# Optimization experiments

Measured on AMD Instinct MI355X. Metric: run time of the kernel, lower is better.

The kernel has to match this reference:

```python
import jax, jax.numpy as jnp
import numpy as np
from jax import lax

B, L, E, K = 16, 512, 512, 3
LOG_SQRT_2PI = 0.5 * float(np.log(2.0 * np.pi))


def conv1d_same(x, w, b):
    # x: (B, L, 1) -> (B, L, E); w: (E, 1, K), same padding for K=3
    y = lax.conv_general_dilated(x.transpose(0, 2, 1), w, (1,), [((K - 1) // 2, (K - 1) // 2)],
                                 dimension_numbers=('NCH', 'OIH', 'NCH'))
    return y.transpose(0, 2, 1) + b


def setup_inputs() -> dict:
    key = jax.random.key(0)
    ks = jax.random.split(key, 12)
    x = jax.random.normal(ks[0], (B, L, E), dtype=jnp.float32)
    durations_int = jax.random.randint(ks[1], (B, L), 1, 9, dtype=jnp.int32)
    durations_float = durations_int.astype(jnp.float32) + 0.1 * jax.random.normal(ks[2], (B, L), dtype=jnp.float32)
    energies = jax.random.normal(ks[3], (B, L), dtype=jnp.float32)
    pitch = jax.random.normal(ks[4], (B, L), dtype=jnp.float32)
    input_lengths = jax.random.randint(ks[5], (B,), 384, 513, dtype=jnp.int32).at[0].set(L)
    # number of frames = max total duration (data-dependent, fixed at setup time)
    T = int(np.max(np.cumsum(np.asarray(durations_int), axis=1)))
    frames_idx = jnp.arange(T, dtype=jnp.float32) + 0.5
    s = 0.02
    w_dur = s * jax.random.normal(ks[6], (E, 1, K), dtype=jnp.float32)
    b_dur = jnp.zeros((E,), dtype=jnp.float32)
    w_nrg = s * jax.random.normal(ks[7], (E, 1, K), dtype=jnp.float32)
    b_nrg = jnp.zeros((E,), dtype=jnp.float32)
    w_pitch = s * jax.random.normal(ks[8], (E, 1, K), dtype=jnp.float32)
    b_pitch = jnp.zeros((E,), dtype=jnp.float32)
    w_proj = s * jax.random.normal(ks[9], (1, E), dtype=jnp.float32)
    b_proj = jnp.zeros((1,), dtype=jnp.float32)
    return dict(x=x, durations_float=durations_float, durations_int=durations_int,
                energies=energies, pitch=pitch, input_lengths=input_lengths,
                frames_idx=frames_idx, w_dur=w_dur, b_dur=b_dur, w_nrg=w_nrg,
                b_nrg=b_nrg, w_pitch=w_pitch, b_pitch=b_pitch, w_proj=w_proj, b_proj=b_proj)


def reference(x, durations_float, durations_int, energies, pitch, input_lengths,
              frames_idx, w_dur, b_dur, w_nrg, b_nrg, w_pitch, b_pitch, w_proj, b_proj):
    dur = conv1d_same(durations_float[..., None], w_dur, b_dur)   # (B,L,E)
    nrg = conv1d_same(energies[..., None], w_nrg, b_nrg)          # (B,L,E)
    pit = conv1d_same(pitch[..., None], w_pitch, b_pitch)         # (B,L,E)
    xc = x + nrg + pit                                            # x_combined == x_summed (no concat)
    range_in = xc + dur
    ranges = jax.nn.softplus(jnp.einsum('ble,oe->blo', range_in, w_proj) + b_proj)[..., 0]  # (B,L)
    pad = jnp.arange(x.shape[1])[None, :] >= input_lengths[:, None]  # True on padded phonemes
    ranges = jnp.clip(jnp.where(pad, 1.0, ranges), 0.001)
    d = durations_int.astype(x.dtype)
    csum = jnp.cumsum(d, axis=1)
    means = d * 0.5 + (csum - d)                                   # center of each phoneme span
    stds = ranges
    # Gaussian log prob over frame centers, (B,L,T)
    z = (frames_idx[None, None, :] - means[..., None]) / stds[..., None]
    probs = jnp.exp(-0.5 * z * z - jnp.log(stds)[..., None] - LOG_SQRT_2PI)
    probs = jnp.where(pad[..., None], 0.0, probs)
    weights = probs / (jnp.sum(probs, axis=1, keepdims=True) + 1e-20)  # normalize over phonemes
    x_upsamp = jnp.einsum('ble,blt->bte', xc, weights)                 # (B,T,E)
    return x_upsamp, weights
```

## Files before the change

### kernel.cpp

```cpp
#include <hip/hip_runtime.h>

typedef unsigned short u16;
typedef unsigned int u32;
typedef __attribute__((ext_vector_type(8))) short short8;
typedef __attribute__((ext_vector_type(4))) float f32x4;

#define LOG_SQRT_2PI 0.9189385332046727f
#define NB 16
#define NL 512
#define NE 512
#define ZWIN 20.0f
#define MAXTB 32

__device__ __forceinline__ u16 f2bf(float x) {
    u32 u = __builtin_bit_cast(u32, x);
    u += 0x7fffu + ((u >> 16) & 1u);
    return (u16)(u >> 16);
}

__device__ __forceinline__ void gload_lds16(const u16* g, u16* l) {
    __builtin_amdgcn_global_load_lds(
        (__attribute__((address_space(1))) void*)(u16*)g,
        (__attribute__((address_space(3))) void*)l,
        16, 0, 0);
}

__global__ void k_xc(const float* __restrict__ x, const float* __restrict__ en,
                     const float* __restrict__ pt,
                     const float* __restrict__ wn, const float* __restrict__ bn,
                     const float* __restrict__ wq, const float* __restrict__ bq,
                     const float* __restrict__ wproj,
                     u16* __restrict__ XcT, float* __restrict__ dot8) {
    __shared__ u16 tile[64][68];
    int b = blockIdx.z;
    int l0 = blockIdx.y * 64, e0 = blockIdx.x * 64;
    int tid = threadIdx.x;
    int c16 = tid & 15, rg = tid >> 4;
    int e = e0 + c16 * 4;
    float wnA[12], wqA[12], bias[4], wp[4];
    {
        const float4* p = (const float4*)(wn + (size_t)e * 3);
        float4 a0 = p[0], a1 = p[1], a2 = p[2];
        wnA[0]=a0.x; wnA[1]=a0.y; wnA[2]=a0.z; wnA[3]=a0.w; wnA[4]=a1.x; wnA[5]=a1.y;
        wnA[6]=a1.z; wnA[7]=a1.w; wnA[8]=a2.x; wnA[9]=a2.y; wnA[10]=a2.z; wnA[11]=a2.w;
        const float4* q = (const float4*)(wq + (size_t)e * 3);
        float4 b0 = q[0], b1 = q[1], b2 = q[2];
        wqA[0]=b0.x; wqA[1]=b0.y; wqA[2]=b0.z; wqA[3]=b0.w; wqA[4]=b1.x; wqA[5]=b1.y;
        wqA[6]=b1.z; wqA[7]=b1.w; wqA[8]=b2.x; wqA[9]=b2.y; wqA[10]=b2.z; wqA[11]=b2.w;
        float4 bn4 = *(const float4*)(bn + e);
        float4 bq4 = *(const float4*)(bq + e);
        bias[0]=bn4.x+bq4.x; bias[1]=bn4.y+bq4.y; bias[2]=bn4.z+bq4.z; bias[3]=bn4.w+bq4.w;
        float4 wp4 = *(const float4*)(wproj + e);
        wp[0]=wp4.x; wp[1]=wp4.y; wp[2]=wp4.z; wp[3]=wp4.w;
    }
    int base = b * NL;
    #pragma unroll
    for (int it = 0; it < 4; ++it) {
        int ll = rg + 16 * it;
        int l = l0 + ll;
        float em1 = (l > 0)   ? en[base + l - 1] : 0.f;
        float ev  = en[base + l];
        float ep1 = (l < 511) ? en[base + l + 1] : 0.f;
        float pm1 = (l > 0)   ? pt[base + l - 1] : 0.f;
        float pv  = pt[base + l];
        float pp1 = (l < 511) ? pt[base + l + 1] : 0.f;
        float4 xv = *(const float4*)(x + ((size_t)(base + l)) * NE + e);
        float xa[4] = {xv.x, xv.y, xv.z, xv.w};
        float pd = 0.f;
        #pragma unroll
        for (int k = 0; k < 4; ++k) {
            float v = xa[k]
                    + wnA[k*3+0] * em1 + wnA[k*3+1] * ev + wnA[k*3+2] * ep1
                    + wqA[k*3+0] * pm1 + wqA[k*3+1] * pv + wqA[k*3+2] * pp1 + bias[k];
            tile[ll][c16 * 4 + k] = f2bf(v);
            pd = fmaf(v, wp[k], pd);
        }
        #pragma unroll
        for (int m = 8; m; m >>= 1) pd += __shfl_xor(pd, m);
        if (c16 == 0) dot8[((size_t)(base + l)) * 8 + blockIdx.x] = pd;
    }
    __syncthreads();
    int lr = tid >> 6, c = tid & 63;
    #pragma unroll 4
    for (int it = 0; it < 16; ++it) {
        int eo = lr + 4 * it;
        XcT[((size_t)b * NE + (e0 + eo)) * NL + l0 + c] = tile[c][eo];
    }
}

__global__ void k_pre(const int* __restrict__ dint, const float* __restrict__ df,
                      const int* __restrict__ lens,
                      const float* __restrict__ wproj, const float* __restrict__ wd,
                      const float* __restrict__ bd, const float* __restrict__ bproj,
                      const float* __restrict__ dot8,
                      float* __restrict__ means, float* __restrict__ inv_std,
                      float* __restrict__ Aarr, int2* __restrict__ win, int ntb) {
    int b = blockIdx.x, l = threadIdx.x;
    __shared__ float s[NL];
    __shared__ float red[4][8];
    __shared__ float tarr[4];
    __shared__ int slo[MAXTB], shi[MAXTB];
    {
        float wp = wproj[l];
        float v[4] = {wp * wd[l * 3 + 0], wp * wd[l * 3 + 1], wp * wd[l * 3 + 2], wp * bd[l]};
        int lane = l & 63, wv = l >> 6;
        #pragma unroll
        for (int i = 0; i < 4; i++) {
            float t = v[i];
            for (int m = 32; m; m >>= 1) t += __shfl_xor(t, m);
            if (lane == 0) red[i][wv] = t;
        }
    }
    if (l < ntb) { slo[l] = NL; shi[l] = -1; }
    float d = (float)dint[b * NL + l];
    s[l] = d;
    __syncthreads();
    if (l < 4) {
        float t = 0.f;
        for (int w2 = 0; w2 < 8; w2++) t += red[l][w2];
        if (l == 3) t += bproj[0];
        tarr[l] = t;
    }
    for (int off = 1; off < NL; off <<= 1) {
        float v = (l >= off) ? s[l - off] : 0.0f;
        __syncthreads();
        s[l] += v;
        __syncthreads();
    }
    float mean = s[l] - 0.5f * d;
    means[b * NL + l] = mean;
    int base = b * NL;
    float dot;
    {
        const float4* dp = (const float4*)(dot8 + ((size_t)(base + l)) * 8);
        float4 a = dp[0], bb4 = dp[1];
        dot = ((a.x + a.y) + (a.z + a.w)) + ((bb4.x + bb4.y) + (bb4.z + bb4.w));
    }
    float dm1 = (l > 0)   ? df[base + l - 1] : 0.f;
    float d0  = df[base + l];
    float dp1 = (l < 511) ? df[base + l + 1] : 0.f;
    float lin = dot + tarr[3]
              + tarr[0] * dm1 + tarr[1] * d0 + tarr[2] * dp1;
    float r = (lin > 20.f) ? lin : log1pf(expf(lin));
    bool pad = (l >= lens[b]);
    if (pad) r = 1.0f;
    float sd = fmaxf(r, 0.001f);
    inv_std[base + l] = 1.0f / sd;
    Aarr[base + l] = pad ? -1e30f : (-logf(sd) - LOG_SQRT_2PI);
    if (!pad) {
        float fl = mean - ZWIN * sd - 1.0f;
        float fh = mean + ZWIN * sd + 1.0f;
        for (int tb = 0; tb < ntb; ++tb) {
            float t_lo = tb * 128.0f + 0.5f, t_hi = tb * 128.0f + 127.5f;
            if (fl <= t_hi && fh >= t_lo) {
                atomicMin(&slo[tb], l);
                atomicMax(&shi[tb], l);
            }
        }
    }
    __syncthreads();
    if (l < ntb) win[b * MAXTB + l] = make_int2(slo[l], shi[l]);
}

__global__ __launch_bounds__(256) void k_gemm(const u16* __restrict__ XcT,
                                              const float* __restrict__ frames,
                                              const float* __restrict__ means,
                                              const float* __restrict__ inv_std,
                                              const float* __restrict__ Aarr,
                                              const int2* __restrict__ win,
                                              float* __restrict__ out,
                                              float* __restrict__ wout, int T) {
    __shared__ float4 sq[NL];
    __shared__ float fts[128];
    __shared__ float part[2][128];
    __shared__ float rvs[128];
    __shared__ u16 At[2][128][32];
    __shared__ u16 Bt[2][128][32];
    int b = blockIdx.z;
    int t0 = blockIdx.y * 128;
    int e0 = blockIdx.x * 128;
    int tid = threadIdx.x;
    int lane = tid & 63, wid = tid >> 6;
    int wm = wid >> 1, wn = wid & 1;
    const u16* Bb = XcT + (size_t)b * NE * NL;

    int2 w = win[b * MAXTB + blockIdx.y];
    int ks0 = 0, nst = 0;
    if (w.x <= w.y) { ks0 = w.x >> 5; nst = (w.y >> 5) - ks0 + 1; }
    int bl0 = ks0 * 32, bl1 = (ks0 + nst) * 32;

    for (int i = bl0 + tid; i < bl1; i += 256)
        sq[i] = make_float4(means[b * NL + i], inv_std[b * NL + i], Aarr[b * NL + i], 0.f);
    if (tid < 128) fts[tid] = (t0 + tid < T) ? frames[t0 + tid] : -1e9f;

    __syncthreads();

    if (nst > 0) {
        int tr = tid & 127, h = tid >> 7;
        float ftr = fts[tr];
        float ssum = 0.f;
        for (int l = w.x + h; l <= w.y; l += 2) {
            float4 q = sq[l];
            float z = (ftr - q.x) * q.y;
            ssum += __expf(fmaf(z, -0.5f * z, q.z));
        }
        part[h][tr] = ssum;
    }
    __syncthreads();
    if (tid < 128) rvs[tid] = 1.0f / (part[0][tid] + part[1][tid] + 1e-20f);
    __syncthreads();

    int ta = tid >> 1;
    int ha = (tid & 1) * 16;
    float ft = fts[ta];
    float rv = rvs[ta];

    int srow = wid * 32 + (lane >> 2);
    int skc = (lane & 3) * 8;

    f32x4 acc[4][4];
    #pragma unroll
    for (int m = 0; m < 4; m++)
        #pragma unroll
        for (int n = 0; n < 4; n++)
            #pragma unroll
            for (int k = 0; k < 4; k++) acc[m][n][k] = 0.0f;

    auto stage = [&](int buf, int ks) {
        int l0 = ks * 32;
        const u16* gb = Bb + (size_t)(e0 + srow) * NL + l0 + skc;
        gload_lds16(gb, &Bt[buf][wid * 32][0]);
        gload_lds16(gb + 16 * NL, &Bt[buf][wid * 32 + 16][0]);
        u32 pk[8];
        #pragma unroll
        for (int jj = 0; jj < 8; ++jj) {
            float4 q0 = sq[l0 + ha + jj * 2];
            float4 q1 = sq[l0 + ha + jj * 2 + 1];
            float z0 = (ft - q0.x) * q0.y;
            float p0 = __expf(fmaf(z0, -0.5f * z0, q0.z)) * rv;
            float z1 = (ft - q1.x) * q1.y;
            float p1 = __expf(fmaf(z1, -0.5f * z1, q1.z)) * rv;
            pk[jj] = (u32)f2bf(p0) | ((u32)f2bf(p1) << 16);
        }
        *(uint4*)&At[buf][ta][ha]     = make_uint4(pk[0], pk[1], pk[2], pk[3]);
        *(uint4*)&At[buf][ta][ha + 8] = make_uint4(pk[4], pk[5], pk[6], pk[7]);
    };

    int fr = lane & 15, fk = (lane >> 4) * 8;
    if (nst > 0) {
        stage(0, ks0);
        for (int s = 0; s < nst; ++s) {
            __syncthreads();
            if (s + 1 < nst) stage((s + 1) & 1, ks0 + s + 1);
            int buf = s & 1;
            short8 a[4], bb[4];
            #pragma unroll
            for (int m = 0; m < 4; m++)
                a[m] = *(const short8*)&At[buf][wm * 64 + m * 16 + fr][fk];
            #pragma unroll
            for (int n = 0; n < 4; n++)
                bb[n] = *(const short8*)&Bt[buf][wn * 64 + n * 16 + fr][fk];
            #pragma unroll
            for (int m = 0; m < 4; m++)
                #pragma unroll
                for (int n = 0; n < 4; n++)
                    acc[m][n] = __builtin_amdgcn_mfma_f32_16x16x32_bf16(a[m], bb[n], acc[m][n], 0, 0, 0);
        }
    }

    int r4 = (lane >> 4) * 4;
    #pragma unroll
    for (int m = 0; m < 4; m++) {
        int tb2 = t0 + wm * 64 + m * 16 + r4;
        #pragma unroll
        for (int j = 0; j < 4; j++) {
            int t = tb2 + j;
            if (t < T) {
                float* orow = out + ((size_t)b * T + t) * NE + e0 + wn * 64 + (lane & 15);
                #pragma unroll
                for (int n = 0; n < 4; n++) orow[n * 16] = acc[m][n][j];
            }
        }
    }

    if (t0 < T) {
        int tcnt = T - t0; if (tcnt > 128) tcnt = 128;
        int rbeg = e0, rend = e0 + 128;
        int ib0 = bl0 > rbeg ? bl0 : rbeg;
        int ib1 = bl1 < rend ? bl1 : rend;
        int t4 = (tid & 31) * 4, rsub = tid >> 5;
        bool t4full = (t4 + 4 <= tcnt);
        float4 z4 = make_float4(0.f, 0.f, 0.f, 0.f);
        auto zfill = [&](int r0, int r1) {
            for (int l = r0 + rsub; l < r1; l += 8) {
                float* d = wout + ((size_t)b * NL + l) * T + t0 + t4;
                if (t4full) *(float4*)d = z4;
                else { for (int u = 0; u < 4 && t4 + u < tcnt; ++u) d[u] = 0.f; }
            }
        };
        if (ib0 >= ib1) {
            zfill(rbeg, rend);
        } else {
            zfill(rbeg, ib0);
            zfill(ib1, rend);
            int tt = tid & 127, half = tid >> 7;
            if (tt < tcnt) {
                float ftl = fts[tt], rvl = rvs[tt];
                float* dstc = wout + (size_t)b * NL * T + t0 + tt;
                for (int l = ib0 + half; l < ib1; l += 2) {
                    float4 q = sq[l];
                    float z = (ftl - q.x) * q.y;
                    dstc[(size_t)l * T] = __expf(fmaf(z, -0.5f * z, q.z)) * rvl;
                }
            }
        }
    }
}

extern "C" void kernel_launch(void* const* d_in, const int* in_sizes, int n_in,
                              void* d_out, int out_size, void* d_ws, size_t ws_size,
                              hipStream_t stream) {
    const float* x      = (const float*)d_in[0];
    const float* df     = (const float*)d_in[1];
    const int*   dint   = (const int*)d_in[2];
    const float* en     = (const float*)d_in[3];
    const float* pt     = (const float*)d_in[4];
    const int*   lens   = (const int*)d_in[5];
    const float* frames = (const float*)d_in[6];
    const float* wd     = (const float*)d_in[7];
    const float* bd     = (const float*)d_in[8];
    const float* wn     = (const float*)d_in[9];
    const float* bn     = (const float*)d_in[10];
    const float* wq     = (const float*)d_in[11];
    const float* bq     = (const float*)d_in[12];
    const float* wproj  = (const float*)d_in[13];
    const float* bproj  = (const float*)d_in[14];

    int T = in_sizes[6];
    int ntb = (T + 127) / 128;

    char* ws = (char*)d_ws;
    float* means   = (float*)(ws);
    float* inv_std = (float*)(ws + 32768);
    float* Aarr    = (float*)(ws + 65536);
    float* dot8    = (float*)(ws + 98304);
    int2*  win     = (int2*)(ws + 360448);
    u16*   XcT     = (u16*)(ws + 364544);

    float* out_up = (float*)d_out;
    float* out_w  = out_up + (size_t)NB * T * NE;

    k_xc<<<dim3(8, 8, NB), dim3(256), 0, stream>>>(x, en, pt, wn, bn, wq, bq, wproj,
                                                   XcT, dot8);
    k_pre<<<dim3(NB), dim3(512), 0, stream>>>(dint, df, lens, wproj, wd, bd, bproj,
                                              dot8, means, inv_std, Aarr, win, ntb);
    k_gemm<<<dim3(4, ntb, NB), dim3(256), 0, stream>>>(XcT, frames, means, inv_std,
                                                       Aarr, win, out_up, out_w, T);
}
```

Baseline: 56.12 us.

## Issue weight-matrix stores before the GEMM loop and split LDS params into arrays

Moves the zero-fill and windowed writes of the normalized weights output ahead of the MFMA main loop, right after the row normalizers are computed. The large global stores can then drain while the tensor-core accumulation runs, instead of forming a store-only tail at the end of each block. It also replaces the float4 per-phoneme parameter array in LDS with three separate float arrays, which shrinks the shared footprint by dropping the unused padding lane. The trade-off is more live state before the GEMM and more separate LDS loads. The old t0<T guard is also dropped on the assumption that the grid never launches blocks past T.

```diff
diff --git a/kernel.cpp b/kernel.cpp
--- a/kernel.cpp
+++ b/kernel.cpp
@@ -170,7 +170,7 @@
                                               const int2* __restrict__ win,
                                               float* __restrict__ out,
                                               float* __restrict__ wout, int T) {
-    __shared__ float4 sq[NL];
+    __shared__ float sm[NL], si[NL], sa[NL];
     __shared__ float fts[128];
     __shared__ float part[2][128];
     __shared__ float rvs[128];
@@ -189,8 +189,30 @@
     if (w.x <= w.y) { ks0 = w.x >> 5; nst = (w.y >> 5) - ks0 + 1; }
     int bl0 = ks0 * 32, bl1 = (ks0 + nst) * 32;
 
-    for (int i = bl0 + tid; i < bl1; i += 256)
-        sq[i] = make_float4(means[b * NL + i], inv_std[b * NL + i], Aarr[b * NL + i], 0.f);
+    int tcnt = T - t0; if (tcnt > 128) tcnt = 128;
+    int rbeg = e0, rend = e0 + 128;
+    int ib0 = bl0 > rbeg ? bl0 : rbeg;
+    int ib1 = bl1 < rend ? bl1 : rend;
+    {
+        int t4 = (tid & 31) * 4, rsub = tid >> 5;
+        bool t4full = (t4 + 4 <= tcnt);
+        float4 z4 = make_float4(0.f, 0.f, 0.f, 0.f);
+        auto zfill = [&](int r0, int r1) {
+            for (int l = r0 + rsub; l < r1; l += 8) {
+                float* d = wout + ((size_t)b * NL + l) * T + t0 + t4;
+                if (t4full) *(float4*)d = z4;
+                else { for (int u = 0; u < 4 && t4 + u < tcnt; ++u) d[u] = 0.f; }
+            }
+        };
+        if (ib0 >= ib1) zfill(rbeg, rend);
+        else { zfill(rbeg, ib0); zfill(ib1, rend); }
+    }
+
+    for (int i = bl0 + tid; i < bl1; i += 256) {
+        sm[i] = means[b * NL + i];
+        si[i] = inv_std[b * NL + i];
+        sa[i] = Aarr[b * NL + i];
+    }
     if (tid < 128) fts[tid] = (t0 + tid < T) ? frames[t0 + tid] : -1e9f;
 
     __syncthreads();
@@ -200,15 +222,26 @@
         float ftr = fts[tr];
         float ssum = 0.f;
         for (int l = w.x + h; l <= w.y; l += 2) {
-            float4 q = sq[l];
-            float z = (ftr - q.x) * q.y;
-            ssum += __expf(fmaf(z, -0.5f * z, q.z));
+            float z = (ftr - sm[l]) * si[l];
+            ssum += __expf(fmaf(z, -0.5f * z, sa[l]));
         }
         part[h][tr] = ssum;
     }
     __syncthreads();
     if (tid < 128) rvs[tid] = 1.0f / (part[0][tid] + part[1][tid] + 1e-20f);
     __syncthreads();
+
+    if (ib0 < ib1) {
+        int tt = tid & 127, half = tid >> 7;
+        if (tt < tcnt) {
+            float ftl = fts[tt], rvl = rvs[tt];
+            float* dstc = wout + (size_t)b * NL * T + t0 + tt;
+            for (int l = ib0 + half; l < ib1; l += 2) {
+                float z = (ftl - sm[l]) * si[l];
+                dstc[(size_t)l * T] = __expf(fmaf(z, -0.5f * z, sa[l])) * rvl;
+            }
+        }
+    }
 
     int ta = tid >> 1;
     int ha = (tid & 1) * 16;
@@ -234,12 +267,11 @@
         u32 pk[8];
         #pragma unroll
         for (int jj = 0; jj < 8; ++jj) {
-            float4 q0 = sq[l0 + ha + jj * 2];
-            float4 q1 = sq[l0 + ha + jj * 2 + 1];
-            float z0 = (ft - q0.x) * q0.y;
-            float p0 = __expf(fmaf(z0, -0.5f * z0, q0.z)) * rv;
-            float z1 = (ft - q1.x) * q1.y;
-            float p1 = __expf(fmaf(z1, -0.5f * z1, q1.z)) * rv;
+            int l0j = l0 + ha + jj * 2;
+            float z0 = (ft - sm[l0j]) * si[l0j];
+            float p0 = __expf(fmaf(z0, -0.5f * z0, sa[l0j])) * rv;
+            float z1 = (ft - sm[l0j + 1]) * si[l0j + 1];
+            float p1 = __expf(fmaf(z1, -0.5f * z1, sa[l0j + 1])) * rv;
             pk[jj] = (u32)f2bf(p0) | ((u32)f2bf(p1) << 16);
         }
         *(uint4*)&At[buf][ta][ha]     = make_uint4(pk[0], pk[1], pk[2], pk[3]);
@@ -282,39 +314,6 @@
             }
         }
     }
-
-    if (t0 < T) {
-        int tcnt = T - t0; if (tcnt > 128) tcnt = 128;
-        int rbeg = e0, rend = e0 + 128;
-        int ib0 = bl0 > rbeg ? bl0 : rbeg;
-        int ib1 = bl1 < rend ? bl1 : rend;
-        int t4 = (tid & 31) * 4, rsub = tid >> 5;
-        bool t4full = (t4 + 4 <= tcnt);
-        float4 z4 = make_float4(0.f, 0.f, 0.f, 0.f);
-        auto zfill = [&](int r0, int r1) {
-            for (int l = r0 + rsub; l < r1; l += 8) {
-                float* d = wout + ((size_t)b * NL + l) * T + t0 + t4;
-                if (t4full) *(float4*)d = z4;
-                else { for (int u = 0; u < 4 && t4 + u < tcnt; ++u) d[u] = 0.f; }
-            }
-        };
-        if (ib0 >= ib1) {
-            zfill(rbeg, rend);
-        } else {
-            zfill(rbeg, ib0);
-            zfill(ib1, rend);
-            int tt = tid & 127, half = tid >> 7;
-            if (tt < tcnt) {
-                float ftl = fts[tt], rvl = rvs[tt];
-                float* dstc = wout + (size_t)b * NL * T + t0 + tt;
-                for (int l = ib0 + half; l < ib1; l += 2) {
-                    float4 q = sq[l];
-                    float z = (ftl - q.x) * q.y;
-                    dstc[(size_t)l * T] = __expf(fmaf(z, -0.5f * z, q.z)) * rvl;
-                }
-            }
-        }
-    }
 }
 
 extern "C" void kernel_launch(void* const* d_in, const int* in_sizes, int n_in,
```

New measurement: 55.22 us. Within noise of the previous version (-1.6%).
